# Kernel optimization log

Hardware: AMD Instinct MI355X
Metric: run time of the kernel (lower is better)

The kernel has to match this reference:

```python
import jax, jax.numpy as jnp
import numpy as np

B, T, D, H = 8, 1024, 1024, 16
HD = D // H  # per-head dim = 64


def setup_inputs() -> dict:
    key = jax.random.key(0)
    ks = jax.random.split(key, 9)
    s = 1.0 / np.sqrt(D)
    return {
        "x": jax.random.normal(ks[0], (B, T, D), dtype=jnp.float32),
        "y": jax.random.normal(ks[1], (B, T, D), dtype=jnp.float32),
        "Wq": jax.random.normal(ks[2], (D, D), dtype=jnp.float32) * s,
        "Wk": jax.random.normal(ks[3], (D, D), dtype=jnp.float32) * s,
        "Wv": jax.random.normal(ks[4], (D, D), dtype=jnp.float32) * s,
        "Wox": jax.random.normal(ks[5], (D, D), dtype=jnp.float32) * s,
        "box": jnp.zeros((D,), dtype=jnp.float32),
        "Woy": jax.random.normal(ks[6], (D, D), dtype=jnp.float32) * s,
        "boy": jnp.zeros((D,), dtype=jnp.float32),
    }


def _split_heads(t):
    # (B, T, D) -> (B, H, T, HD)
    return t.reshape(B, T, H, HD).transpose(0, 2, 1, 3)


def _merge_heads(t):
    # (B, H, T, HD) -> (B, T, D)
    return t.transpose(0, 2, 1, 3).reshape(B, T, D)


def reference(x, y, Wq, Wk, Wv, Wox, box, Woy, boy):
    # Shared Q/K/V projections applied cross-wise (torch Linear: t @ W.T)
    q_sx = _split_heads(y @ Wq.T)  # queries from y attend over x
    k_sx = _split_heads(x @ Wk.T)
    v_sx = _split_heads(x @ Wv.T)
    q_sy = _split_heads(x @ Wq.T)  # queries from x attend over y
    k_sy = _split_heads(y @ Wk.T)
    v_sy = _split_heads(y @ Wv.T)

    scale = jnp.sqrt(jnp.asarray(HD, dtype=x.dtype))
    scores_x = jnp.einsum('bhqd,bhkd->bhqk', q_sx, k_sx)
    scores_y = jnp.einsum('bhqd,bhkd->bhqk', q_sy, k_sy)
    # cat on head dim + reshape(B,2,H,T,T) + mean over dim 1 == per-head average
    attn = jax.nn.softmax((scores_x + scores_y) * (0.5 / scale), axis=-1)

    out1 = _merge_heads(jnp.einsum('bhqk,bhkd->bhqd', attn, v_sx))
    out2 = _merge_heads(jnp.einsum('bhqk,bhkd->bhqd', attn, v_sy))
    out1 = out1 @ Wox.T + box
    out2 = out2 @ Woy.T + boy
    return (out1, out2)
```

## Files before the change

### kernel.cpp

```cpp
#include <hip/hip_runtime.h>
#include <stdint.h>

#define DEV __device__ __forceinline__

typedef __bf16 bf16x8 __attribute__((ext_vector_type(8)));
typedef float f32x4 __attribute__((ext_vector_type(4)));
typedef unsigned short u16;
typedef u16 u16x4v __attribute__((ext_vector_type(4)));
typedef u16 u16x8 __attribute__((ext_vector_type(8)));
typedef uint32_t u32;

static constexpr int Bb = 8, Tt = 1024, Dd = 1024, Hh = 16;
static constexpr int BT = Bb * Tt;

DEV u16 f2bf(float f) {
  u32 u = __float_as_uint(f);
  u32 r = (u + 0x7FFFu + ((u >> 16) & 1u)) >> 16;
  return (u16)r;
}
DEV u32 pack2(float a, float b) {
  return (u32)f2bf(a) | ((u32)f2bf(b) << 16);
}
DEV void gload_lds16(const void* g, void* lds) {
  __builtin_amdgcn_global_load_lds(
      (const __attribute__((address_space(1))) void*)g,
      (__attribute__((address_space(3))) void*)lds,
      16, 0, 0);
}

__global__ __launch_bounds__(256) void k_cvt2(const float* __restrict__ x,
                                              const float* __restrict__ y,
                                              u16* __restrict__ xb, u16* __restrict__ yb) {
  const float* src = blockIdx.z ? y : x;
  u16* dst = blockIdx.z ? yb : xb;
  const int n8 = BT * Dd / 8;
  int i = blockIdx.x * blockDim.x + threadIdx.x;
  int stride = gridDim.x * blockDim.x;
  for (; i < n8; i += stride) {
    const float4* p = reinterpret_cast<const float4*>(src) + (size_t)i * 2;
    float4 a = p[0], b = p[1];
    u16x8 o;
    o[0] = f2bf(a.x); o[1] = f2bf(a.y); o[2] = f2bf(a.z); o[3] = f2bf(a.w);
    o[4] = f2bf(b.x); o[5] = f2bf(b.y); o[6] = f2bf(b.z); o[7] = f2bf(b.w);
    reinterpret_cast<u16x8*>(dst)[i] = o;
  }
}

__global__ __launch_bounds__(256) void k_cvt5(const float* __restrict__ a0,
                                              const float* __restrict__ a1,
                                              const float* __restrict__ a2,
                                              const float* __restrict__ a3,
                                              const float* __restrict__ a4,
                                              u16* __restrict__ Wb) {
  int z = blockIdx.z;
  const float* src = (z == 0) ? a0 : (z == 1) ? a1 : (z == 2) ? a2 : (z == 3) ? a3 : a4;
  u16* dst = Wb + (size_t)z * (Dd * Dd);
  int i = blockIdx.x * blockDim.x + threadIdx.x;
  const float4* p = reinterpret_cast<const float4*>(src) + (size_t)i * 2;
  float4 a = p[0], b = p[1];
  u16x8 o;
  o[0] = f2bf(a.x); o[1] = f2bf(a.y); o[2] = f2bf(a.z); o[3] = f2bf(a.w);
  o[4] = f2bf(b.x); o[5] = f2bf(b.y); o[6] = f2bf(b.z); o[7] = f2bf(b.w);
  reinterpret_cast<u16x8*>(dst)[i] = o;
}

template <int MODE, int GX, int GY>
__global__ __launch_bounds__(512, 2) void k_gemm256(
    const u16* __restrict__ xb, const u16* __restrict__ yb,
    const u16* __restrict__ W0,
    u16* __restrict__ Qb, u16* __restrict__ Kb, u16* __restrict__ Vtg,
    const float* __restrict__ bx, const float* __restrict__ by,
    float* __restrict__ out) {
  __shared__ alignas(16) u16 As[2][256 * 64];
  __shared__ alignas(16) u16 Bs[2][256 * 64];
  const int tid = threadIdx.x;
  const int l = tid & 63, wid = tid >> 6;
  const int wr = wid >> 2, wc = wid & 3;

  constexpr int NWG = GX * GY * 2;
  const int d0b = blockIdx.x;
  const int wk = (d0b & 7) * (NWG / 8) + (d0b >> 3);
  const int tz = wk / (GX * GY);
  const int rr = wk % (GX * GY);
  const int ty = rr / GX, tx = rr % GX;
  const int m0 = ty * 256, n0 = tx * 256;

  const u16* Ag;
  const u16* Wg;
  if constexpr (MODE == 0) {
    Ag = tz ? yb : xb;
    Wg = W0;
  } else {
    Ag = xb + tz * 64;
    Wg = W0 + (size_t)tz * (Dd * Dd);
  }

  auto stageA = [&](int buf, int kt, int half) {
#pragma unroll
    for (int i = 0; i < 2; ++i) {
      int idx = i * 512 + tid;
      int row = idx >> 3, P = idx & 7, G = P ^ (row & 7);
      const u16* src;
      if constexpr (MODE == 0) {
        src = Ag + (size_t)(m0 + half * 128 + row) * 1024 + kt * 64 + G * 8;
      } else {
        int m = m0 + half * 128 + row;
        src = Ag + ((size_t)((m >> 10) * 16 + kt) * 1024 + (m & 1023)) * 128 + G * 8;
      }
      gload_lds16(src, &As[buf][half * 8192 + idx * 8]);
    }
  };
  auto stageB = [&](int buf, int kt, int half) {
#pragma unroll
    for (int i = 0; i < 2; ++i) {
      int idx = i * 512 + tid;
      int row = idx >> 3, P = idx & 7, G = P ^ (row & 7);
      gload_lds16(Wg + (size_t)(n0 + half * 128 + row) * 1024 + kt * 64 + G * 8,
                  &Bs[buf][half * 8192 + idx * 8]);
    }
  };
  auto ldA = [&](int b, int m, int kk) -> bf16x8 {
    int row = wr * 128 + m * 16 + (l & 15);
    int P = (kk * 4 + (l >> 4)) ^ (row & 7);
    return *reinterpret_cast<const bf16x8*>(&As[b][row * 64 + P * 8]);
  };
  auto ldB = [&](int b, int n, int kk) -> bf16x8 {
    int row = wc * 64 + n * 16 + (l & 15);
    int P = (kk * 4 + (l >> 4)) ^ (row & 7);
    return *reinterpret_cast<const bf16x8*>(&Bs[b][row * 64 + P * 8]);
  };

  f32x4 acc[8][4] = {};

  stageA(0, 0, 0); stageB(0, 0, 0); stageA(0, 0, 1); stageB(0, 0, 1);
  asm volatile("s_waitcnt vmcnt(0)" ::: "memory");
  __builtin_amdgcn_s_barrier();

  for (int kt = 0; kt < 16; ++kt) {
    const int b = kt & 1, nb = b ^ 1;
    const bool pf = (kt < 15);
    bf16x8 bfr[4][2], afr[2][2];

#define QUAD(p)                                                                     \
  do {                                                                              \
    __builtin_amdgcn_s_barrier();                                                   \
    asm volatile("s_waitcnt lgkmcnt(0)" ::: "memory");                              \
    __builtin_amdgcn_sched_barrier(0);                                              \
    __builtin_amdgcn_s_setprio(1);                                                  \
    _Pragma("unroll") for (int mm = 0; mm < 2; ++mm)                                \
        _Pragma("unroll") for (int n = 0; n < 4; ++n)                               \
            _Pragma("unroll") for (int kk = 0; kk < 2; ++kk)                        \
                acc[2 * (p) + mm][n] = __builtin_amdgcn_mfma_f32_16x16x32_bf16(     \
                    afr[mm][kk], bfr[n][kk], acc[2 * (p) + mm][n], 0, 0, 0);        \
    __builtin_amdgcn_s_setprio(0);                                                  \
  } while (0)

#pragma unroll
    for (int n = 0; n < 4; ++n) { bfr[n][0] = ldB(b, n, 0); bfr[n][1] = ldB(b, n, 1); }
    afr[0][0] = ldA(b, 0, 0); afr[0][1] = ldA(b, 0, 1);
    afr[1][0] = ldA(b, 1, 0); afr[1][1] = ldA(b, 1, 1);
    if (pf) { stageA(nb, kt + 1, 0); stageB(nb, kt + 1, 0); }
    QUAD(0);
    __builtin_amdgcn_s_barrier();

    afr[0][0] = ldA(b, 2, 0); afr[0][1] = ldA(b, 2, 1);
    afr[1][0] = ldA(b, 3, 0); afr[1][1] = ldA(b, 3, 1);
    if (pf) { stageA(nb, kt + 1, 1); stageB(nb, kt + 1, 1); }
    QUAD(1);
    __builtin_amdgcn_s_barrier();

    afr[0][0] = ldA(b, 4, 0); afr[0][1] = ldA(b, 4, 1);
    afr[1][0] = ldA(b, 5, 0); afr[1][1] = ldA(b, 5, 1);
    QUAD(2);
    __builtin_amdgcn_s_barrier();

    afr[0][0] = ldA(b, 6, 0); afr[0][1] = ldA(b, 6, 1);
    afr[1][0] = ldA(b, 7, 0); afr[1][1] = ldA(b, 7, 1);
    QUAD(3);
    asm volatile("s_waitcnt vmcnt(0)" ::: "memory");
    __builtin_amdgcn_s_barrier();
#undef QUAD
  }

#pragma unroll
  for (int m = 0; m < 8; ++m)
#pragma unroll
    for (int n = 0; n < 4; ++n) {
      int rb = m0 + wr * 128 + m * 16 + (l >> 4) * 4;
      int col = n0 + wc * 64 + n * 16 + (l & 15);
      if constexpr (MODE == 0) {
        int proj = col >> 10;
        int slot = ((proj == 0) ? 1 : 0) ^ tz;
        int bh = ((rb >> 10) << 4) + ((col >> 6) & 15);
        int t0 = rb & 1023;
        int dc = col & 63;
        if (proj == 2) {
          u16x4v pk;
#pragma unroll
          for (int j = 0; j < 4; ++j) pk[j] = f2bf(acc[m][n][j]);
          *reinterpret_cast<u16x4v*>(Vtg + (size_t)bh * 131072 +
                                     (size_t)(slot * 64 + dc) * 1024 + t0) = pk;
        } else {
          float sc = (proj == 0) ? 0.0625f : 1.0f;
          u16* dstp = (proj ? Kb : Qb) + (size_t)bh * 131072 + (size_t)t0 * 128 + slot * 64 + dc;
#pragma unroll
          for (int j = 0; j < 4; ++j) dstp[(size_t)j * 128] = f2bf(acc[m][n][j] * sc);
        }
      } else {
        const float* bias = tz ? by : bx;
        float* dstp = out + (size_t)tz * BT * Dd;
        float bv = bias[col];
#pragma unroll
        for (int j = 0; j < 4; ++j)
          dstp[(size_t)(rb + j) * 1024 + col] = acc[m][n][j] + bv;
      }
    }
}

__global__ __launch_bounds__(256) void k_attn(const u16* __restrict__ Q,
                                              const u16* __restrict__ K,
                                              const u16* __restrict__ Vt,
                                              u16* __restrict__ O) {
  __shared__ alignas(16) u16 Ks[64 * 128];
  __shared__ alignas(16) u16 Vs[128 * 64];
  const int tid = threadIdx.x;
  const int l = tid & 63, w = tid >> 6;
  const int bid = blockIdx.x;
  const int xcd = bid & 7, li = bid >> 3;
  const int bh = xcd + 8 * (li >> 4);
  const int qx = li & 15;
  const int q0 = qx * 64 + w * 16;
  const size_t base = (size_t)bh * 131072;

  bf16x8 qf[4];
#pragma unroll
  for (int dc = 0; dc < 4; ++dc)
    qf[dc] = *reinterpret_cast<const bf16x8*>(
        Q + base + (size_t)(q0 + (l & 15)) * 128 + dc * 32 + (l >> 4) * 8);

  float m_run = -3e38f, l_run = 0.f;
  f32x4 Oa[8] = {};

  for (int kv0 = 0; kv0 < 1024; kv0 += 64) {
#pragma unroll
    for (int rep = 0; rep < 4; ++rep) {
      int chunk = rep * 4 + w;
      int idx = chunk * 64 + l;
      {
        int row = idx >> 4, P = idx & 15, G = P ^ (row & 7);
        gload_lds16(K + base + (size_t)(kv0 + row) * 128 + G * 8, &Ks[chunk * 512]);
      }
      {
        int d = idx >> 3, p = idx & 7, g = p ^ (d & 7);
        gload_lds16(Vt + base + (size_t)d * 1024 + kv0 + g * 8, &Vs[chunk * 512]);
      }
    }
    __syncthreads();

    f32x4 S[4];
    __builtin_amdgcn_s_setprio(1);
#pragma unroll
    for (int t = 0; t < 4; ++t) {
      f32x4 s = {};
      int row = t * 16 + (l & 15);
#pragma unroll
      for (int dc = 0; dc < 4; ++dc) {
        int P = (dc * 4 + (l >> 4)) ^ (row & 7);
        bf16x8 kb = *reinterpret_cast<const bf16x8*>(&Ks[row * 128 + P * 8]);
        s = __builtin_amdgcn_mfma_f32_16x16x32_bf16(kb, qf[dc], s, 0, 0, 0);
      }
      S[t] = s;
    }
    __builtin_amdgcn_s_setprio(0);

    float mx = S[0][0];
#pragma unroll
    for (int t = 0; t < 4; ++t)
#pragma unroll
      for (int j = 0; j < 4; ++j) mx = fmaxf(mx, S[t][j]);
    mx = fmaxf(mx, __shfl_xor(mx, 16));
    mx = fmaxf(mx, __shfl_xor(mx, 32));
    float mn = fmaxf(m_run, mx);
    float alpha = __expf(m_run - mn);
    m_run = mn;
    float p[4][4];
    float rs = 0.f;
#pragma unroll
    for (int t = 0; t < 4; ++t)
#pragma unroll
      for (int j = 0; j < 4; ++j) {
        p[t][j] = __expf(S[t][j] - mn);
        rs += p[t][j];
      }
    rs += __shfl_xor(rs, 16);
    rs += __shfl_xor(rs, 32);
    l_run = alpha * l_run + rs;

    u32 u[4][2];
#pragma unroll
    for (int t = 0; t < 4; ++t) {
      u[t][0] = pack2(p[t][0], p[t][1]);
      u[t][1] = pack2(p[t][2], p[t][3]);
    }

    {
      f32x4 av;
#pragma unroll
      for (int j = 0; j < 4; ++j) av[j] = __shfl(alpha, (l >> 4) * 4 + j);
#pragma unroll
      for (int n = 0; n < 8; ++n) Oa[n] *= av;
    }

    const bool hi = (l >= 32);
    const int srcA = (l & 15) + ((l >> 4) & 1) * 32;
#pragma unroll
    for (int c = 0; c < 2; ++c) {
      u32 r0a = __shfl(u[2 * c][0], srcA),      r0b = __shfl(u[2 * c + 1][0], srcA);
      u32 r1a = __shfl(u[2 * c][1], srcA),      r1b = __shfl(u[2 * c + 1][1], srcA);
      u32 r2a = __shfl(u[2 * c][0], srcA + 16), r2b = __shfl(u[2 * c + 1][0], srcA + 16);
      u32 r3a = __shfl(u[2 * c][1], srcA + 16), r3b = __shfl(u[2 * c + 1][1], srcA + 16);
      union { u32 wd[4]; bf16x8 v; } pu;
      pu.wd[0] = hi ? r0b : r0a;
      pu.wd[1] = hi ? r1b : r1a;
      pu.wd[2] = hi ? r2b : r2a;
      pu.wd[3] = hi ? r3b : r3a;
      bf16x8 pa = pu.v;
      __builtin_amdgcn_s_setprio(1);
#pragma unroll
      for (int n = 0; n < 8; ++n) {
        int d = n * 16 + (l & 15);
        int pp = (c * 4 + (l >> 4)) ^ (d & 7);
        bf16x8 vb = *reinterpret_cast<const bf16x8*>(&Vs[d * 64 + pp * 8]);
        Oa[n] = __builtin_amdgcn_mfma_f32_16x16x32_bf16(pa, vb, Oa[n], 0, 0, 0);
      }
      __builtin_amdgcn_s_setprio(0);
    }
    __syncthreads();
  }

  float inv = 1.0f / l_run;
  f32x4 iv;
#pragma unroll
  for (int j = 0; j < 4; ++j) iv[j] = __shfl(inv, (l >> 4) * 4 + j);
#pragma unroll
  for (int n = 0; n < 8; ++n)
#pragma unroll
    for (int j = 0; j < 4; ++j)
      O[base + (size_t)(q0 + (l >> 4) * 4 + j) * 128 + n * 16 + (l & 15)] = f2bf(Oa[n][j] * iv[j]);
}

extern "C" void kernel_launch(void* const* d_in, const int* in_sizes, int n_in,
                              void* d_out, int out_size, void* d_ws, size_t ws_size,
                              hipStream_t stream) {
  const float* x   = (const float*)d_in[0];
  const float* y   = (const float*)d_in[1];
  const float* Wq  = (const float*)d_in[2];
  const float* Wk  = (const float*)d_in[3];
  const float* Wv  = (const float*)d_in[4];
  const float* Wox = (const float*)d_in[5];
  const float* box = (const float*)d_in[6];
  const float* Woy = (const float*)d_in[7];
  const float* boy = (const float*)d_in[8];

  u16* ws = (u16*)d_ws;
  size_t off = 0;
  u16* xb  = ws + off; off += (size_t)BT * Dd;
  u16* yb  = ws + off; off += (size_t)BT * Dd;
  u16* Wqb = ws + off; off += (size_t)Dd * Dd;
  u16* Wkb = ws + off; off += (size_t)Dd * Dd;
  u16* Wvb = ws + off; off += (size_t)Dd * Dd;
  u16* Woxb = ws + off; off += (size_t)Dd * Dd;
  u16* Woyb = ws + off; off += (size_t)Dd * Dd;
  (void)Wkb; (void)Wvb; (void)Woyb;
  const size_t attn_elems = (size_t)Bb * Hh * Tt * 128;
  u16* Qb = ws + off; off += attn_elems;
  u16* Kb = ws + off; off += attn_elems;
  u16* Vb = ws + off; off += attn_elems;
  u16* Ob = ws + off; off += attn_elems;

  k_cvt2<<<dim3(1024, 1, 2), dim3(256), 0, stream>>>(x, y, xb, yb);
  k_cvt5<<<dim3(512, 1, 5), dim3(256), 0, stream>>>(Wq, Wk, Wv, Wox, Woy, Wqb);

  k_gemm256<0, 12, 32><<<dim3(768), dim3(512), 0, stream>>>(
      xb, yb, Wqb, Qb, Kb, Vb, nullptr, nullptr, nullptr);

  k_attn<<<dim3(2048), dim3(256), 0, stream>>>(Qb, Kb, Vb, Ob);

  k_gemm256<1, 4, 32><<<dim3(256), dim3(512), 0, stream>>>(
      Ob, nullptr, Woxb, nullptr, nullptr, nullptr, box, boy, (float*)d_out);
}
```

Before: 302.5 us.

## Restructure attention inner loop: transposed PV MFMA, exp2 softmax, lazy rescale, new LDS layout

```diff
diff --git a/kernel.cpp b/kernel.cpp
--- a/kernel.cpp
+++ b/kernel.cpp
@@ -4,6 +4,8 @@
 #define DEV __device__ __forceinline__
 
 typedef __bf16 bf16x8 __attribute__((ext_vector_type(8)));
+typedef __bf16 bf16x4 __attribute__((ext_vector_type(4)));
+typedef short s16x4 __attribute__((ext_vector_type(4)));
 typedef float f32x4 __attribute__((ext_vector_type(4)));
 typedef unsigned short u16;
 typedef u16 u16x4v __attribute__((ext_vector_type(4)));
@@ -18,14 +20,28 @@
   u32 r = (u + 0x7FFFu + ((u >> 16) & 1u)) >> 16;
   return (u16)r;
 }
-DEV u32 pack2(float a, float b) {
-  return (u32)f2bf(a) | ((u32)f2bf(b) << 16);
+DEV u32 cvtpk(float lo, float hi) {
+  u32 r;
+  asm("v_cvt_pk_bf16_f32 %0, %1, %2" : "=v"(r) : "v"(lo), "v"(hi));
+  return r;
 }
 DEV void gload_lds16(const void* g, void* lds) {
   __builtin_amdgcn_global_load_lds(
       (const __attribute__((address_space(1))) void*)g,
       (__attribute__((address_space(3))) void*)lds,
       16, 0, 0);
+}
+DEV f32x4 MFMA16(bf16x4 a, bf16x4 b, f32x4 c) {
+#if __has_builtin(__builtin_amdgcn_mfma_f32_16x16x16_bf16)
+  return __builtin_amdgcn_mfma_f32_16x16x16_bf16(a, b, c, 0, 0, 0);
+#elif __has_builtin(__builtin_amdgcn_mfma_f32_16x16x16bf16_1k)
+  union { bf16x4 b; s16x4 s; } ua, ub;
+  ua.b = a; ub.b = b;
+  return __builtin_amdgcn_mfma_f32_16x16x16bf16_1k(ua.s, ub.s, c, 0, 0, 0);
+#else
+  asm("v_mfma_f32_16x16x16_bf16 %0, %1, %2, %0" : "+v"(c) : "v"(a), "v"(b));
+  return c;
+#endif
 }
 
 __global__ __launch_bounds__(256) void k_cvt2(const float* __restrict__ x,
@@ -195,13 +211,14 @@
         int t0 = rb & 1023;
         int dc = col & 63;
         if (proj == 2) {
+          int newoff = (t0 >> 5) * 32 + ((t0 >> 2) & 3) * 8 + ((t0 >> 4) & 1) * 4;
           u16x4v pk;
 #pragma unroll
           for (int j = 0; j < 4; ++j) pk[j] = f2bf(acc[m][n][j]);
           *reinterpret_cast<u16x4v*>(Vtg + (size_t)bh * 131072 +
-                                     (size_t)(slot * 64 + dc) * 1024 + t0) = pk;
+                                     (size_t)(slot * 64 + dc) * 1024 + newoff) = pk;
         } else {
-          float sc = (proj == 0) ? 0.0625f : 1.0f;
+          float sc = (proj == 0) ? 0.09016994f : 1.0f;
           u16* dstp = (proj ? Kb : Qb) + (size_t)bh * 131072 + (size_t)t0 * 128 + slot * 64 + dc;
 #pragma unroll
           for (int j = 0; j < 4; ++j) dstp[(size_t)j * 128] = f2bf(acc[m][n][j] * sc);
@@ -221,8 +238,8 @@
                                               const u16* __restrict__ K,
                                               const u16* __restrict__ Vt,
                                               u16* __restrict__ O) {
-  __shared__ alignas(16) u16 Ks[64 * 128];
-  __shared__ alignas(16) u16 Vs[128 * 64];
+  __shared__ alignas(16) u16 Ks[4 * 64 * 32];
+  __shared__ alignas(16) u16 Vs[2 * 128 * 32];
   const int tid = threadIdx.x;
   const int l = tid & 63, w = tid >> 6;
   const int bid = blockIdx.x;
@@ -238,22 +255,32 @@
     qf[dc] = *reinterpret_cast<const bf16x8*>(
         Q + base + (size_t)(q0 + (l & 15)) * 128 + dc * 32 + (l >> 4) * 8);
 
+  const u16* kp[4];
+  const u16* vp[4];
+#pragma unroll
+  for (int r = 0; r < 4; ++r) {
+    int idx = (r * 4 + w) * 64 + l;
+    {
+      int dc = idx >> 8, kv = (idx >> 2) & 63, pp = idx & 3, g = pp ^ ((kv >> 1) & 3);
+      kp[r] = K + base + (size_t)kv * 128 + dc * 32 + g * 8;
+    }
+    {
+      int c = idx >> 9, d = (idx >> 2) & 127, pp = idx & 3, g = pp ^ ((d >> 1) & 3);
+      vp[r] = Vt + base + (size_t)d * 1024 + c * 32 + g * 8;
+    }
+  }
+  const int koff = (l & 15) * 32 + (((l >> 4) ^ (((l & 15) >> 1) & 3))) * 8;
+  const int voff = koff;
+
   float m_run = -3e38f, l_run = 0.f;
   f32x4 Oa[8] = {};
 
   for (int kv0 = 0; kv0 < 1024; kv0 += 64) {
 #pragma unroll
-    for (int rep = 0; rep < 4; ++rep) {
-      int chunk = rep * 4 + w;
-      int idx = chunk * 64 + l;
-      {
-        int row = idx >> 4, P = idx & 15, G = P ^ (row & 7);
-        gload_lds16(K + base + (size_t)(kv0 + row) * 128 + G * 8, &Ks[chunk * 512]);
-      }
-      {
-        int d = idx >> 3, p = idx & 7, g = p ^ (d & 7);
-        gload_lds16(Vt + base + (size_t)d * 1024 + kv0 + g * 8, &Vs[chunk * 512]);
-      }
+    for (int r = 0; r < 4; ++r) {
+      int chunk = r * 4 + w;
+      gload_lds16(kp[r] + (size_t)kv0 * 128, &Ks[chunk * 512 + l * 8]);
+      gload_lds16(vp[r] + kv0, &Vs[chunk * 512 + l * 8]);
     }
     __syncthreads();
 
@@ -262,91 +289,78 @@
 #pragma unroll
     for (int t = 0; t < 4; ++t) {
       f32x4 s = {};
-      int row = t * 16 + (l & 15);
 #pragma unroll
       for (int dc = 0; dc < 4; ++dc) {
-        int P = (dc * 4 + (l >> 4)) ^ (row & 7);
-        bf16x8 kb = *reinterpret_cast<const bf16x8*>(&Ks[row * 128 + P * 8]);
+        bf16x8 kb = *reinterpret_cast<const bf16x8*>(&Ks[dc * 2048 + t * 512 + koff]);
         s = __builtin_amdgcn_mfma_f32_16x16x32_bf16(kb, qf[dc], s, 0, 0, 0);
       }
       S[t] = s;
     }
     __builtin_amdgcn_s_setprio(0);
 
-    float mx = S[0][0];
-#pragma unroll
-    for (int t = 0; t < 4; ++t)
-#pragma unroll
-      for (int j = 0; j < 4; ++j) mx = fmaxf(mx, S[t][j]);
+    float mx = fmaxf(fmaxf(fmaxf(S[0][0], S[0][1]), fmaxf(S[0][2], S[0][3])),
+                     fmaxf(fmaxf(S[1][0], S[1][1]), fmaxf(S[1][2], S[1][3])));
+    float mx2 = fmaxf(fmaxf(fmaxf(S[2][0], S[2][1]), fmaxf(S[2][2], S[2][3])),
+                      fmaxf(fmaxf(S[3][0], S[3][1]), fmaxf(S[3][2], S[3][3])));
+    mx = fmaxf(mx, mx2);
     mx = fmaxf(mx, __shfl_xor(mx, 16));
     mx = fmaxf(mx, __shfl_xor(mx, 32));
-    float mn = fmaxf(m_run, mx);
-    float alpha = __expf(m_run - mn);
-    m_run = mn;
-    float p[4][4];
+
+    const int grow = __any(mx > m_run + 11.0f);
+    float mn = grow ? fmaxf(m_run, mx) : m_run;
     float rs = 0.f;
 #pragma unroll
     for (int t = 0; t < 4; ++t)
 #pragma unroll
       for (int j = 0; j < 4; ++j) {
-        p[t][j] = __expf(S[t][j] - mn);
-        rs += p[t][j];
+        S[t][j] = __builtin_exp2f(S[t][j] - mn);
+        rs += S[t][j];
       }
     rs += __shfl_xor(rs, 16);
     rs += __shfl_xor(rs, 32);
-    l_run = alpha * l_run + rs;
-
-    u32 u[4][2];
+    if (grow) {
+      float alpha = __builtin_exp2f(m_run - mn);
+      m_run = mn;
+      l_run = alpha * l_run + rs;
+#pragma unroll
+      for (int n = 0; n < 8; ++n) Oa[n] *= alpha;
+    } else {
+      l_run += rs;
+    }
+
+    union { u32 w2[2]; bf16x4 v; } pb[4];
 #pragma unroll
     for (int t = 0; t < 4; ++t) {
-      u[t][0] = pack2(p[t][0], p[t][1]);
-      u[t][1] = pack2(p[t][2], p[t][3]);
-    }
-
-    {
-      f32x4 av;
-#pragma unroll
-      for (int j = 0; j < 4; ++j) av[j] = __shfl(alpha, (l >> 4) * 4 + j);
-#pragma unroll
-      for (int n = 0; n < 8; ++n) Oa[n] *= av;
-    }
-
-    const bool hi = (l >= 32);
-    const int srcA = (l & 15) + ((l >> 4) & 1) * 32;
-#pragma unroll
-    for (int c = 0; c < 2; ++c) {
-      u32 r0a = __shfl(u[2 * c][0], srcA),      r0b = __shfl(u[2 * c + 1][0], srcA);
-      u32 r1a = __shfl(u[2 * c][1], srcA),      r1b = __shfl(u[2 * c + 1][1], srcA);
-      u32 r2a = __shfl(u[2 * c][0], srcA + 16), r2b = __shfl(u[2 * c + 1][0], srcA + 16);
-      u32 r3a = __shfl(u[2 * c][1], srcA + 16), r3b = __shfl(u[2 * c + 1][1], srcA + 16);
-      union { u32 wd[4]; bf16x8 v; } pu;
-      pu.wd[0] = hi ? r0b : r0a;
-      pu.wd[1] = hi ? r1b : r1a;
-      pu.wd[2] = hi ? r2b : r2a;
-      pu.wd[3] = hi ? r3b : r3a;
-      bf16x8 pa = pu.v;
-      __builtin_amdgcn_s_setprio(1);
+      pb[t].w2[0] = cvtpk(S[t][0], S[t][1]);
+      pb[t].w2[1] = cvtpk(S[t][2], S[t][3]);
+    }
+
+    asm volatile("s_nop 1");
+    __builtin_amdgcn_s_setprio(1);
+#pragma unroll
+    for (int c = 0; c < 2; ++c)
 #pragma unroll
       for (int n = 0; n < 8; ++n) {
-        int d = n * 16 + (l & 15);
-        int pp = (c * 4 + (l >> 4)) ^ (d & 7);
-        bf16x8 vb = *reinterpret_cast<const bf16x8*>(&Vs[d * 64 + pp * 8]);
-        Oa[n] = __builtin_amdgcn_mfma_f32_16x16x32_bf16(pa, vb, Oa[n], 0, 0, 0);
+        bf16x8 av = *reinterpret_cast<const bf16x8*>(&Vs[c * 4096 + n * 512 + voff]);
+        bf16x4 a0 = __builtin_shufflevector(av, av, 0, 1, 2, 3);
+        bf16x4 a1 = __builtin_shufflevector(av, av, 4, 5, 6, 7);
+        Oa[n] = MFMA16(a0, pb[2 * c].v, Oa[n]);
+        Oa[n] = MFMA16(a1, pb[2 * c + 1].v, Oa[n]);
       }
-      __builtin_amdgcn_s_setprio(0);
-    }
+    __builtin_amdgcn_s_setprio(0);
     __syncthreads();
   }
+  asm volatile("s_nop 7");
 
   float inv = 1.0f / l_run;
-  f32x4 iv;
-#pragma unroll
-  for (int j = 0; j < 4; ++j) iv[j] = __shfl(inv, (l >> 4) * 4 + j);
-#pragma unroll
-  for (int n = 0; n < 8; ++n)
-#pragma unroll
-    for (int j = 0; j < 4; ++j)
-      O[base + (size_t)(q0 + (l >> 4) * 4 + j) * 128 + n * 16 + (l & 15)] = f2bf(Oa[n][j] * iv[j]);
+#pragma unroll
+  for (int n = 0; n < 8; ++n) {
+    u16x4v pk;
+#pragma unroll
+    for (int j = 0; j < 4; ++j) pk[j] = f2bf(Oa[n][j] * inv);
+    *reinterpret_cast<u16x4v*>(
+        O + base + (size_t)(q0 + (l & 15)) * 128 + n * 16 + (l >> 4) * 4) = pk;
+  }
 }
 
 extern "C" void kernel_launch(void* const* d_in, const int* in_sizes, int n_in,
```

New measurement: 292.8 us. 3.2% less time.
